# Optimization experiments

Hardware: AMD Instinct MI355X
Metric: run time of the kernel (lower is better)

The kernel has to match this reference:

```python
import jax, jax.numpy as jnp
import numpy as np

NUM_CHARTS = 16
LATENT_DIM = 128
RANK = 128
BATCH = 131072


def _init_weight(key, out_dim, in_dim):
    # nn.init.eye_ on top-left block, then += 0.01 * randn (identity-ish init)
    w = jnp.zeros((out_dim, in_dim), jnp.float32)
    m = min(out_dim, in_dim)
    w = w.at[jnp.arange(m), jnp.arange(m)].set(1.0)
    return w + 0.01 * jax.random.normal(key, (out_dim, in_dim), jnp.float32)


def setup_inputs() -> dict:
    key = jax.random.key(0)
    ks = jax.random.split(key, 3 + 2 * NUM_CHARTS)
    z_n = jax.random.normal(ks[0], (BATCH, LATENT_DIM), jnp.float32)
    source_idx = jax.random.randint(ks[1], (BATCH,), 0, NUM_CHARTS, dtype=jnp.int64 if jax.config.jax_enable_x64 else jnp.int32)
    target_idx = jax.random.randint(ks[2], (BATCH,), 0, NUM_CHARTS, dtype=source_idx.dtype)
    # encoder weights: [C, R, D] (torch Linear weight layout [out, in])
    enc_w = jnp.stack([_init_weight(ks[3 + i], RANK, LATENT_DIM) for i in range(NUM_CHARTS)])
    # decoder weights: [C, D, R]
    dec_w = jnp.stack([_init_weight(ks[3 + NUM_CHARTS + i], LATENT_DIM, RANK) for i in range(NUM_CHARTS)])
    c_param = jnp.zeros((NUM_CHARTS, RANK), jnp.float32)
    d_param = jnp.zeros((NUM_CHARTS, LATENT_DIM), jnp.float32)
    return {"z_n": z_n, "source_idx": source_idx, "target_idx": target_idx,
            "enc_w": enc_w, "dec_w": dec_w, "c_param": c_param, "d_param": d_param}


def _apply_per_chart(x, chart_idx, weights):
    # x: [B, in], weights: [C, out, in] -> [B, out]
    # Loop over the small fixed chart count; each chart does one dense GEMM,
    # results routed by mask-select (same math as gather/compute/scatter).
    C = weights.shape[0]
    out = jnp.zeros((x.shape[0], weights.shape[1]), x.dtype)
    for c in range(C):
        yc = x @ weights[c].T  # [B, out]
        out = jnp.where((chart_idx == c)[:, None], yc, out)
    return out


def reference(z_n, source_idx, target_idx, enc_w, dec_w, c_param, d_param):
    # lift_to_global: per-chart encode + bias c[src]
    h = _apply_per_chart(z_n, source_idx, enc_w) + c_param[source_idx]  # [B, R]
    # project_from_global: per-chart decode + bias d[tgt]
    z_out = _apply_per_chart(h, target_idx, dec_w) + d_param[target_idx]  # [B, D]
    return z_out
```

## Files before the change

kernel.cpp:

```cpp
#include <hip/hip_runtime.h>
#include <hip/hip_bf16.h>

#define NB     131072
#define NCH    16
#define NPAIR  256
#define LDW    136
#define LDH    136
#define LDO    132

#define WS_HIST   0
#define WS_OFF    256
#define WS_SORTED 528
#define WS_BYTES  ((WS_SORTED + NB) * 4)

typedef short short8 __attribute__((ext_vector_type(8)));
typedef float f32x4  __attribute__((ext_vector_type(4)));

__device__ __forceinline__ short bfbits(float x) {
    union { __hip_bfloat16 h; short s; } u;
    u.h = __float2bfloat16(x);
    return u.s;
}

__device__ __forceinline__ short8 cvt_frag(const float* __restrict__ p) {
    const f32x4 lo = *(const f32x4*)p;
    const f32x4 hi = *(const f32x4*)(p + 4);
    short8 r;
    r[0] = bfbits(lo[0]); r[1] = bfbits(lo[1]); r[2] = bfbits(lo[2]); r[3] = bfbits(lo[3]);
    r[4] = bfbits(hi[0]); r[5] = bfbits(hi[1]); r[6] = bfbits(hi[2]); r[7] = bfbits(hi[3]);
    return r;
}

__global__ void k_init(int* __restrict__ hist) {
    hist[threadIdx.x] = 0;
}

__global__ __launch_bounds__(256) void k_hist(const int* __restrict__ si,
                                              const int* __restrict__ ti,
                                              int* __restrict__ hist) {
    __shared__ int sh[NPAIR];
    const int t = threadIdx.x;
    sh[t] = 0;
    __syncthreads();
    const int base = blockIdx.x * 2048 + t;
#pragma unroll
    for (int j = 0; j < 8; ++j) {
        const int i = base + j * 256;
        const int k = (si[i] * NCH + ti[i]) & (NPAIR - 1);
        atomicAdd(&sh[k], 1);
    }
    __syncthreads();
    if (sh[t]) atomicAdd(&hist[t], sh[t]);
}

__global__ __launch_bounds__(256) void k_scan(int* __restrict__ hist,
                                              int* __restrict__ off) {
    __shared__ int s[NPAIR];
    const int t = threadIdx.x;
    const int v = hist[t];
    s[t] = v;
    __syncthreads();
#pragma unroll
    for (int d = 1; d < NPAIR; d <<= 1) {
        const int x = (t >= d) ? s[t - d] : 0;
        __syncthreads();
        s[t] += x;
        __syncthreads();
    }
    off[t + 1] = s[t];
    if (t == 0) off[0] = 0;
    hist[t] = s[t] - v;
}

__global__ __launch_bounds__(256) void k_scatter(const int* __restrict__ si,
                                                 const int* __restrict__ ti,
                                                 int* __restrict__ cursor,
                                                 int* __restrict__ sorted) {
    __shared__ int sh[NPAIR];
    __shared__ int sbase[NPAIR];
    const int t = threadIdx.x;
    sh[t] = 0;
    __syncthreads();
    int key[8], rank[8];
    const int base = blockIdx.x * 2048 + t;
#pragma unroll
    for (int j = 0; j < 8; ++j) {
        const int i = base + j * 256;
        const int k = (si[i] * NCH + ti[i]) & (NPAIR - 1);
        key[j]  = k;
        rank[j] = atomicAdd(&sh[k], 1);
    }
    __syncthreads();
    sbase[t] = sh[t] ? atomicAdd(&cursor[t], sh[t]) : 0;
    __syncthreads();
#pragma unroll
    for (int j = 0; j < 8; ++j) {
        const int slot = sbase[key[j]] + rank[j];
        if (slot >= 0 && slot < NB)
            sorted[slot] = base + j * 256;
    }
}

__global__ __launch_bounds__(256, 1)
void k_gemm(const float* __restrict__ z,
            const float* __restrict__ encw,
            const float* __restrict__ decw,
            const float* __restrict__ cpar,
            const float* __restrict__ dpar,
            const int* __restrict__ off,
            const int* __restrict__ sorted,
            float* __restrict__ out) {
    __shared__ int sRow[128];
    __shared__ __align__(16) __hip_bfloat16 sW1[128 * LDW];
    __shared__ __align__(16) __hip_bfloat16 sW2[128 * LDW];
    __shared__ __align__(16) float sOut[128 * LDO];
    __hip_bfloat16* const sH = (__hip_bfloat16*)sOut;

    const int bucket = blockIdx.x;
    const int srcc = bucket >> 4;
    const int tgtc = bucket & (NCH - 1);
    const int beg = off[bucket];
    const int end = off[bucket + 1];

    const int tid  = threadIdx.x;
    const int lane = tid & 63;
    const int wv   = tid >> 6;
    const int lr   = lane & 15;
    const int lhi  = lane >> 4;
    const int mb   = wv * 32;

    {
        const float* W1 = encw + srcc * 16384;
        const float* W2 = decw + tgtc * 16384;
#pragma unroll
        for (int it = 0; it < 8; ++it) {
            const int f = (it * 256 + tid) * 8;
            const int row = f >> 7, col = f & 127;
            *(short8*)(sW1 + row * LDW + col) = cvt_frag(W1 + f);
            *(short8*)(sW2 + row * LDW + col) = cvt_frag(W2 + f);
        }
    }
    __syncthreads();

    short8 b1[8][4];
#pragma unroll
    for (int nt = 0; nt < 8; ++nt)
#pragma unroll
        for (int k = 0; k < 4; ++k)
            b1[nt][k] = *(const short8*)(sW1 + (nt * 16 + lr) * LDW + k * 32 + lhi * 8);

    float cb[8], db[8];
#pragma unroll
    for (int nt = 0; nt < 8; ++nt) {
        cb[nt] = cpar[srcc * 128 + nt * 16 + lr];
        db[nt] = dpar[tgtc * 128 + nt * 16 + lr];
    }

    const int ntile = (end - beg + 127) >> 7;
    for (int tile = 0; tile < ntile; ++tile) {
        const int rbeg = beg + tile * 128;
        __syncthreads();
        if (tid < 128) {
            const int g = rbeg + tid;
            int v = (g < end) ? sorted[g] : -1;
            sRow[tid] = ((unsigned)v < (unsigned)NB) ? v : -1;
        }
        __syncthreads();

        const int r0 = sRow[mb + lr];
        const int r1 = sRow[mb + 16 + lr];
        const float* pz0 = z + (long)(r0 < 0 ? 0 : r0) * 128 + lhi * 8;
        const float* pz1 = z + (long)(r1 < 0 ? 0 : r1) * 128 + lhi * 8;

        f32x4 acc[2][8];
#pragma unroll
        for (int mt = 0; mt < 2; ++mt)
#pragma unroll
            for (int nt = 0; nt < 8; ++nt) acc[mt][nt] = (f32x4)(0.0f);

#pragma unroll
        for (int k = 0; k < 4; ++k) {
            const short8 a0 = cvt_frag(pz0 + k * 32);
            const short8 a1 = cvt_frag(pz1 + k * 32);
#pragma unroll
            for (int nt = 0; nt < 8; ++nt) {
                acc[0][nt] = __builtin_amdgcn_mfma_f32_16x16x32_bf16(a0, b1[nt][k], acc[0][nt], 0, 0, 0);
                acc[1][nt] = __builtin_amdgcn_mfma_f32_16x16x32_bf16(a1, b1[nt][k], acc[1][nt], 0, 0, 0);
            }
        }

#pragma unroll
        for (int nt = 0; nt < 8; ++nt)
#pragma unroll
            for (int mt = 0; mt < 2; ++mt) {
                const int row = mb + mt * 16 + lhi * 4;
                const int col = nt * 16 + lr;
#pragma unroll
                for (int r = 0; r < 4; ++r)
                    sH[(row + r) * LDH + col] = __float2bfloat16(acc[mt][nt][r] + cb[nt]);
            }
        __syncthreads();

#pragma unroll
        for (int mt = 0; mt < 2; ++mt)
#pragma unroll
            for (int nt = 0; nt < 8; ++nt) acc[mt][nt] = (f32x4)(0.0f);

#pragma unroll
        for (int k = 0; k < 4; ++k) {
            const short8 a0 = *(const short8*)(sH + (mb + lr) * LDH + k * 32 + lhi * 8);
            const short8 a1 = *(const short8*)(sH + (mb + 16 + lr) * LDH + k * 32 + lhi * 8);
#pragma unroll
            for (int nt = 0; nt < 8; ++nt) {
                const short8 b = *(const short8*)(sW2 + (nt * 16 + lr) * LDW + k * 32 + lhi * 8);
                acc[0][nt] = __builtin_amdgcn_mfma_f32_16x16x32_bf16(a0, b, acc[0][nt], 0, 0, 0);
                acc[1][nt] = __builtin_amdgcn_mfma_f32_16x16x32_bf16(a1, b, acc[1][nt], 0, 0, 0);
            }
        }
        __syncthreads();

#pragma unroll
        for (int nt = 0; nt < 8; ++nt)
#pragma unroll
            for (int mt = 0; mt < 2; ++mt) {
                const int row = mb + mt * 16 + lhi * 4;
                const int col = nt * 16 + lr;
#pragma unroll
                for (int r = 0; r < 4; ++r)
                    sOut[(row + r) * LDO + col] = acc[mt][nt][r] + db[nt];
            }
        __syncthreads();

        {
            const int rr0 = tid >> 5;
            const int c4  = (tid & 31) * 4;
#pragma unroll
            for (int it = 0; it < 16; ++it) {
                const int rr = rr0 + it * 8;
                const int grow = sRow[rr];
                if (grow >= 0)
                    *(f32x4*)(out + (long)grow * 128 + c4) =
                        *(const f32x4*)(sOut + rr * LDO + c4);
            }
        }
    }
}

__global__ __launch_bounds__(256)
void k_fallback(const float* __restrict__ z,
                const int* __restrict__ si, const int* __restrict__ ti,
                const float* __restrict__ ew,
                const float* __restrict__ dw,
                const float* __restrict__ cp,
                const float* __restrict__ dp,
                float* __restrict__ out) {
    __shared__ float sh[4][128];
    const int lane = threadIdx.x & 63, wv = threadIdx.x >> 6;
    for (int row = blockIdx.x * 4 + wv; row < NB; row += (int)gridDim.x * 4) {
        const int sc = si[row] & (NCH - 1), tc = ti[row] & (NCH - 1);
        const float* zr = z + (long)row * 128;
        const float* W1 = ew + sc * 16384;
        float h0 = cp[sc * 128 + lane];
        float h1 = cp[sc * 128 + lane + 64];
        for (int d = 0; d < 128; ++d) {
            const float zv = zr[d];
            h0 += zv * W1[lane * 128 + d];
            h1 += zv * W1[(lane + 64) * 128 + d];
        }
        sh[wv][lane] = h0;
        sh[wv][lane + 64] = h1;
        __syncthreads();
        const float* W2 = dw + tc * 16384;
        float o0 = dp[tc * 128 + lane];
        float o1 = dp[tc * 128 + lane + 64];
        for (int r = 0; r < 128; ++r) {
            const float hv = sh[wv][r];
            o0 += hv * W2[lane * 128 + r];
            o1 += hv * W2[(lane + 64) * 128 + r];
        }
        out[(long)row * 128 + lane] = o0;
        out[(long)row * 128 + lane + 64] = o1;
        __syncthreads();
    }
}

extern "C" void kernel_launch(void* const* d_in, const int* in_sizes, int n_in,
                              void* d_out, int out_size, void* d_ws, size_t ws_size,
                              hipStream_t stream) {
    const float* z  = (const float*)d_in[0];
    const int*   si = (const int*)d_in[1];
    const int*   ti = (const int*)d_in[2];
    const float* ew = (const float*)d_in[3];
    const float* dw = (const float*)d_in[4];
    const float* cp = (const float*)d_in[5];
    const float* dp = (const float*)d_in[6];
    float* out = (float*)d_out;

    if (ws_size >= (size_t)WS_BYTES) {
        int* hist   = (int*)d_ws + WS_HIST;
        int* off    = (int*)d_ws + WS_OFF;
        int* sorted = (int*)d_ws + WS_SORTED;

        k_init<<<1, NPAIR, 0, stream>>>(hist);
        k_hist<<<64, 256, 0, stream>>>(si, ti, hist);
        k_scan<<<1, NPAIR, 0, stream>>>(hist, off);
        k_scatter<<<64, 256, 0, stream>>>(si, ti, hist, sorted);
        k_gemm<<<NPAIR, 256, 0, stream>>>(z, ew, dw, cp, dp, off, sorted, out);
    } else {
        k_fallback<<<1024, 256, 0, stream>>>(z, si, ti, ew, dw, cp, dp, out);
    }
}
```

Before: 162.3 us.

## Fuse histogram, scan, scatter and grouped GEMM into one cooperative kernel

Replaces the five-kernel pipeline (init, histogram, scan, scatter, grouped GEMM) with a single cooperative-launch kernel that uses grid-wide syncs between the bucketing phases. It then runs the per-pair two-stage bf16 MFMA GEMM, splitting each of the 256 (source, target) buckets across two blocks, for 512 blocks in total. The aim is to remove launch gaps and the separate small kernels. In exchange it adds a memset launch, three grid barriers and a residency requirement of two blocks per CU. It also keeps the first-layer weights in registers, which could raise register pressure.

```diff
diff --git a/kernel.cpp b/kernel.cpp
--- a/kernel.cpp
+++ b/kernel.cpp
@@ -1,5 +1,8 @@
 #include <hip/hip_runtime.h>
 #include <hip/hip_bf16.h>
+#include <hip/hip_cooperative_groups.h>
+
+namespace cg = cooperative_groups;
 
 #define NB     131072
 #define NCH    16
@@ -7,6 +10,8 @@
 #define LDW    136
 #define LDH    136
 #define LDO    132
+#define GRID_F 512
+#define RPB    (NB / GRID_F)
 
 #define WS_HIST   0
 #define WS_OFF    256
@@ -29,6 +34,178 @@
     r[0] = bfbits(lo[0]); r[1] = bfbits(lo[1]); r[2] = bfbits(lo[2]); r[3] = bfbits(lo[3]);
     r[4] = bfbits(hi[0]); r[5] = bfbits(hi[1]); r[6] = bfbits(hi[2]); r[7] = bfbits(hi[3]);
     return r;
+}
+
+__global__ __launch_bounds__(256, 2)
+void k_fused(const float* __restrict__ z,
+             const int* __restrict__ si,
+             const int* __restrict__ ti,
+             const float* __restrict__ encw,
+             const float* __restrict__ decw,
+             const float* __restrict__ cpar,
+             const float* __restrict__ dpar,
+             int* __restrict__ hist,
+             int* __restrict__ cursor,
+             int* __restrict__ sorted,
+             float* __restrict__ out) {
+    __shared__ int sh[NPAIR];
+    __shared__ int sAux[NPAIR];
+    __shared__ int soff[NPAIR + 1];
+    __shared__ int sRow[128];
+    __shared__ __align__(16) __hip_bfloat16 sW2[128 * LDW];
+    __shared__ __align__(16) __hip_bfloat16 sH[128 * LDH];
+
+    const int tid = threadIdx.x;
+    const int bid = blockIdx.x;
+    cg::grid_group grid = cg::this_grid();
+
+    sh[tid] = 0;
+    __syncthreads();
+    const int row = bid * RPB + tid;
+    const int key = (si[row] * NCH + ti[row]) & (NPAIR - 1);
+    const int rank = atomicAdd(&sh[key], 1);
+    __syncthreads();
+    const int cnt = sh[tid];
+    if (cnt) atomicAdd(&hist[tid], cnt);
+    grid.sync();
+
+    const int v = __hip_atomic_load(&hist[tid], __ATOMIC_RELAXED, __HIP_MEMORY_SCOPE_AGENT);
+    sAux[tid] = v;
+    __syncthreads();
+#pragma unroll
+    for (int d = 1; d < NPAIR; d <<= 1) {
+        const int x = (tid >= d) ? sAux[tid - d] : 0;
+        __syncthreads();
+        sAux[tid] += x;
+        __syncthreads();
+    }
+    soff[tid + 1] = sAux[tid];
+    if (tid == 0) soff[0] = 0;
+    if (bid == 0) cursor[tid] = sAux[tid] - v;
+    grid.sync();
+
+    sAux[tid] = cnt ? atomicAdd(&cursor[tid], cnt) : 0;
+    __syncthreads();
+    const int slot = sAux[key] + rank;
+    if ((unsigned)slot < (unsigned)NB) sorted[slot] = row;
+    __threadfence();
+    const int bucket = bid >> 1;
+    const int half   = bid & 1;
+    const int beg = soff[bucket];
+    const int end = soff[bucket + 1];
+    grid.sync();
+
+    const int srcc = bucket >> 4;
+    const int tgtc = bucket & (NCH - 1);
+    const int lane = tid & 63;
+    const int wv   = tid >> 6;
+    const int lr   = lane & 15;
+    const int lhi  = lane >> 4;
+    const int mb   = wv * 32;
+
+    {
+        const float* W1 = encw + srcc * 16384;
+        const float* W2 = decw + tgtc * 16384;
+#pragma unroll
+        for (int it = 0; it < 8; ++it) {
+            const int f = (it * 256 + tid) * 8;
+            const int r_ = f >> 7, c_ = f & 127;
+            *(short8*)(sH  + r_ * LDH + c_) = cvt_frag(W1 + f);
+            *(short8*)(sW2 + r_ * LDW + c_) = cvt_frag(W2 + f);
+        }
+    }
+    __syncthreads();
+
+    short8 b1[8][4];
+#pragma unroll
+    for (int nt = 0; nt < 8; ++nt)
+#pragma unroll
+        for (int k = 0; k < 4; ++k)
+            b1[nt][k] = *(const short8*)(sH + (nt * 16 + lr) * LDH + k * 32 + lhi * 8);
+
+    float cb[8], db[8];
+#pragma unroll
+    for (int nt = 0; nt < 8; ++nt) {
+        cb[nt] = cpar[srcc * 128 + nt * 16 + lr];
+        db[nt] = dpar[tgtc * 128 + nt * 16 + lr];
+    }
+
+    const int ntile = (end - beg + 127) >> 7;
+    for (int tile = half; tile < ntile; tile += 2) {
+        const int rbeg = beg + tile * 128;
+        __syncthreads();
+        if (tid < 128) {
+            const int g = rbeg + tid;
+            int vv = (g < end) ? sorted[g] : -1;
+            sRow[tid] = ((unsigned)vv < (unsigned)NB) ? vv : -1;
+        }
+        __syncthreads();
+
+        const int r0 = sRow[mb + lr];
+        const int r1 = sRow[mb + 16 + lr];
+        const float* pz0 = z + (long)(r0 < 0 ? 0 : r0) * 128 + lhi * 8;
+        const float* pz1 = z + (long)(r1 < 0 ? 0 : r1) * 128 + lhi * 8;
+
+        f32x4 acc[2][8];
+#pragma unroll
+        for (int mt = 0; mt < 2; ++mt)
+#pragma unroll
+            for (int nt = 0; nt < 8; ++nt) acc[mt][nt] = (f32x4)(0.0f);
+
+#pragma unroll
+        for (int k = 0; k < 4; ++k) {
+            const short8 a0 = cvt_frag(pz0 + k * 32);
+            const short8 a1 = cvt_frag(pz1 + k * 32);
+#pragma unroll
+            for (int nt = 0; nt < 8; ++nt) {
+                acc[0][nt] = __builtin_amdgcn_mfma_f32_16x16x32_bf16(a0, b1[nt][k], acc[0][nt], 0, 0, 0);
+                acc[1][nt] = __builtin_amdgcn_mfma_f32_16x16x32_bf16(a1, b1[nt][k], acc[1][nt], 0, 0, 0);
+            }
+        }
+
+#pragma unroll
+        for (int nt = 0; nt < 8; ++nt)
+#pragma unroll
+            for (int mt = 0; mt < 2; ++mt) {
+                const int rowb = mb + mt * 16 + lhi * 4;
+                const int col = nt * 16 + lr;
+#pragma unroll
+                for (int r = 0; r < 4; ++r)
+                    sH[(rowb + r) * LDH + col] = __float2bfloat16(acc[mt][nt][r] + cb[nt]);
+            }
+        __syncthreads();
+
+#pragma unroll
+        for (int mt = 0; mt < 2; ++mt)
+#pragma unroll
+            for (int nt = 0; nt < 8; ++nt) acc[mt][nt] = (f32x4)(0.0f);
+
+#pragma unroll
+        for (int k = 0; k < 4; ++k) {
+            const short8 a0 = *(const short8*)(sH + (mb + lr) * LDH + k * 32 + lhi * 8);
+            const short8 a1 = *(const short8*)(sH + (mb + 16 + lr) * LDH + k * 32 + lhi * 8);
+#pragma unroll
+            for (int nt = 0; nt < 8; ++nt) {
+                const short8 b = *(const short8*)(sW2 + (nt * 16 + lr) * LDW + k * 32 + lhi * 8);
+                acc[0][nt] = __builtin_amdgcn_mfma_f32_16x16x32_bf16(a0, b, acc[0][nt], 0, 0, 0);
+                acc[1][nt] = __builtin_amdgcn_mfma_f32_16x16x32_bf16(a1, b, acc[1][nt], 0, 0, 0);
+            }
+        }
+
+#pragma unroll
+        for (int mt = 0; mt < 2; ++mt) {
+            const int rb = mb + mt * 16 + lhi * 4;
+            int gr[4];
+#pragma unroll
+            for (int r = 0; r < 4; ++r) gr[r] = sRow[rb + r];
+#pragma unroll
+            for (int nt = 0; nt < 8; ++nt)
+#pragma unroll
+                for (int r = 0; r < 4; ++r)
+                    if (gr[r] >= 0)
+                        out[(long)gr[r] * 128 + nt * 16 + lr] = acc[mt][nt][r] + db[nt];
+        }
+    }
 }
 
 __global__ void k_init(int* __restrict__ hist) {
@@ -298,14 +475,36 @@
 
     if (ws_size >= (size_t)WS_BYTES) {
         int* hist   = (int*)d_ws + WS_HIST;
-        int* off    = (int*)d_ws + WS_OFF;
+        int* curoff = (int*)d_ws + WS_OFF;
         int* sorted = (int*)d_ws + WS_SORTED;
+
+        static int coopChecked = 0, coopOK = 0;
+        if (!coopChecked) {
+            coopChecked = 1;
+            int dev = 0;
+            (void)hipGetDevice(&dev);
+            (void)hipDeviceGetAttribute(&coopOK, hipDeviceAttributeCooperativeLaunch, dev);
+        }
+
+        if (coopOK) {
+            (void)hipMemsetAsync(hist, 0, NPAIR * sizeof(int), stream);
+            void* args[] = {
+                (void*)&z, (void*)&si, (void*)&ti, (void*)&ew, (void*)&dw,
+                (void*)&cp, (void*)&dp, (void*)&hist, (void*)&curoff,
+                (void*)&sorted, (void*)&out
+            };
+            hipError_t e = hipLaunchCooperativeKernel((const void*)k_fused,
+                                                      dim3(GRID_F), dim3(256),
+                                                      args, 0, stream);
+            if (e == hipSuccess) return;
+            (void)hipGetLastError();
+        }
 
         k_init<<<1, NPAIR, 0, stream>>>(hist);
         k_hist<<<64, 256, 0, stream>>>(si, ti, hist);
-        k_scan<<<1, NPAIR, 0, stream>>>(hist, off);
+        k_scan<<<1, NPAIR, 0, stream>>>(hist, curoff);
         k_scatter<<<64, 256, 0, stream>>>(si, ti, hist, sorted);
-        k_gemm<<<NPAIR, 256, 0, stream>>>(z, ew, dw, cp, dp, off, sorted, out);
+        k_gemm<<<NPAIR, 256, 0, stream>>>(z, ew, dw, cp, dp, curoff, sorted, out);
     } else {
         k_fallback<<<1024, 256, 0, stream>>>(z, si, ti, ew, dw, cp, dp, out);
     }
```

Result: slower. 378.7 us (+133.3%).
